# Optimization experiments

Measured on AMD Instinct MI355X. Metric: run time of the kernel, lower is better.

## Reference

```python
import jax, jax.numpy as jnp
import numpy as np

B, L, D, H = 8, 2048, 1024, 16
FACTOR = 3


def setup_inputs() -> dict:
    key = jax.random.key(0)
    ks = jax.random.split(key, 11)
    s = 0.02
    mk = lambda k, shp: jax.random.normal(k, shp, dtype=jnp.float32)
    return {
        "queries": mk(ks[0], (B, L, D)),
        "keys": mk(ks[1], (B, L, D)),
        "values": mk(ks[2], (B, L, D)),
        "Wq": mk(ks[3], (D, D)) * s, "bq": jnp.zeros((D,), jnp.float32),
        "Wk": mk(ks[4], (D, D)) * s, "bk": jnp.zeros((D,), jnp.float32),
        "Wv": mk(ks[5], (D, D)) * s, "bv": jnp.zeros((D,), jnp.float32),
        "Wo": mk(ks[6], (D, D)) * s, "bo": jnp.zeros((D,), jnp.float32),
    }


def reference(queries, keys, values, Wq, bq, Wk, bk, Wv, bv, Wo, bo):
    b, length, d = queries.shape
    h = H
    e = d // h
    q = (queries @ Wq + bq).reshape(b, length, h, e)
    k = (keys @ Wk + bk).reshape(b, length, h, e)
    v = (values @ Wv + bv).reshape(b, length, h, e)

    # [B, H, E, L] layout for FFT along time
    qf = jnp.fft.rfft(q.transpose(0, 2, 3, 1), axis=-1)
    kf = jnp.fft.rfft(k.transpose(0, 2, 3, 1), axis=-1)
    corr = jnp.fft.irfft(qf * jnp.conj(kf), n=length, axis=-1)  # [B,H,E,L]

    vperm = v.transpose(0, 2, 3, 1)  # [B,H,E,L]
    top_k = int(FACTOR * np.log(length))  # static: 22 for L=2048
    weights, delay = jax.lax.top_k(corr, top_k)          # [B,H,E,K]
    temp_corr = jax.nn.softmax(weights, axis=-1)         # [B,H,E,K]

    idx0 = jnp.arange(length)  # [L]
    agg = jnp.zeros_like(vperm)
    # small fixed loop over top-k delays (mirrors original structure)
    for i in range(top_k):
        # faithful to source: indices wrapped mod 8 (original code quirk)
        td = (idx0[None, None, None, :] + delay[..., i:i + 1]) % 8  # [B,H,E,L]
        pattern = jnp.take_along_axis(vperm, td, axis=-1)
        agg = agg + pattern * temp_corr[..., i:i + 1]

    result = agg.transpose(0, 3, 1, 2).reshape(b, length, d)  # [B,L,D]
    out = result @ Wo + bo
    return (out, corr.transpose(0, 3, 1, 2))
```

## Files before the change

### kernel.cpp

```cpp
#include <hip/hip_runtime.h>
#include <cstdint>
#include <cstddef>


#define TOPK 22

typedef __attribute__((ext_vector_type(8))) short short8;
typedef __attribute__((ext_vector_type(4))) float f32x4;

__device__ __forceinline__ float bf2f(unsigned short u) {
  union { unsigned int i; float f; } w;
  w.i = ((unsigned int)u) << 16;
  return w.f;
}
__device__ __forceinline__ unsigned short f2bf(float f) {
  union { float f; unsigned int i; } w;
  w.f = f;
  unsigned int x = w.i;
  x += 0x7fffu + ((x >> 16) & 1u);
  return (unsigned short)(x >> 16);
}

__device__ __forceinline__ float2 make2(float x, float y) { float2 r; r.x = x; r.y = y; return r; }
__device__ __forceinline__ float2 cadd(float2 a, float2 b) { return make2(a.x + b.x, a.y + b.y); }
__device__ __forceinline__ float2 csub(float2 a, float2 b) { return make2(a.x - b.x, a.y - b.y); }
__device__ __forceinline__ float2 cmul(float2 a, float2 b) {
  return make2(a.x * b.x - a.y * b.y, a.x * b.y + a.y * b.x);
}

__device__ __forceinline__ int cfi(int u) { return 2 * u + (((u) >> 5) << 1); }

template <bool INV>
__device__ __forceinline__ void dft8(float2 (&v)[8]) {
  const float C = 0.70710678118654752f;
  float2 s0 = cadd(v[0], v[4]), s1 = csub(v[0], v[4]);
  float2 s2 = cadd(v[2], v[6]), s3 = csub(v[2], v[6]);
  float2 E0 = cadd(s0, s2), E2 = csub(s0, s2);
  float2 E1, E3;
  if (!INV) { E1 = make2(s1.x + s3.y, s1.y - s3.x); E3 = make2(s1.x - s3.y, s1.y + s3.x); }
  else      { E1 = make2(s1.x - s3.y, s1.y + s3.x); E3 = make2(s1.x + s3.y, s1.y - s3.x); }
  float2 q0 = cadd(v[1], v[5]), q1 = csub(v[1], v[5]);
  float2 q2 = cadd(v[3], v[7]), q3 = csub(v[3], v[7]);
  float2 O0 = cadd(q0, q2), O2 = csub(q0, q2);
  float2 O1, O3;
  if (!INV) { O1 = make2(q1.x + q3.y, q1.y - q3.x); O3 = make2(q1.x - q3.y, q1.y + q3.x); }
  else      { O1 = make2(q1.x - q3.y, q1.y + q3.x); O3 = make2(q1.x + q3.y, q1.y - q3.x); }
  float2 T0 = O0, T1, T2, T3;
  if (!INV) {
    T1 = make2(C * (O1.x + O1.y), C * (O1.y - O1.x));
    T2 = make2(O2.y, -O2.x);
    T3 = make2(C * (O3.y - O3.x), -C * (O3.x + O3.y));
  } else {
    T1 = make2(C * (O1.x - O1.y), C * (O1.x + O1.y));
    T2 = make2(-O2.y, O2.x);
    T3 = make2(-C * (O3.x + O3.y), C * (O3.x - O3.y));
  }
  v[0] = cadd(E0, T0); v[4] = csub(E0, T0);
  v[1] = cadd(E1, T1); v[5] = csub(E1, T1);
  v[2] = cadd(E2, T2); v[6] = csub(E2, T2);
  v[3] = cadd(E3, T3); v[7] = csub(E3, T3);
}

template <bool INV>
__device__ __forceinline__ void dft4(float2 (&v)[4]) {
  float2 s0 = cadd(v[0], v[2]), s1 = csub(v[0], v[2]);
  float2 s2 = cadd(v[1], v[3]), s3 = csub(v[1], v[3]);
  v[0] = cadd(s0, s2); v[2] = csub(s0, s2);
  if (!INV) { v[1] = make2(s1.x + s3.y, s1.y - s3.x); v[3] = make2(s1.x - s3.y, s1.y + s3.x); }
  else      { v[1] = make2(s1.x - s3.y, s1.y + s3.x); v[3] = make2(s1.x + s3.y, s1.y - s3.x); }
}

template <int NS, bool INV>
__device__ __forceinline__ void stage8(const float* __restrict__ src,
                                       float* __restrict__ dst, int tid) {
  float2 v[8];
#pragma unroll
  for (int m = 0; m < 8; ++m)
    v[m] = *reinterpret_cast<const float2*>(src + cfi(tid + (m << 8)));
  if constexpr (NS > 1) {
    const int r = tid & (NS - 1);
    const float rev = (INV ? (1.0f / (8 * NS)) : (-1.0f / (8 * NS))) * (float)r;
    float2 w1; w1.x = __builtin_amdgcn_cosf(rev); w1.y = __builtin_amdgcn_sinf(rev);
    const float2 w2 = cmul(w1, w1);
    const float2 w3 = cmul(w2, w1);
    const float2 w4 = cmul(w2, w2);
    const float2 w5 = cmul(w4, w1);
    const float2 w6 = cmul(w4, w2);
    const float2 w7 = cmul(w4, w3);
    v[1] = cmul(v[1], w1); v[2] = cmul(v[2], w2); v[3] = cmul(v[3], w3);
    v[4] = cmul(v[4], w4); v[5] = cmul(v[5], w5); v[6] = cmul(v[6], w6);
    v[7] = cmul(v[7], w7);
  }
  dft8<INV>(v);
  const int r2 = tid & (NS - 1);
  const int d = ((tid & ~(NS - 1)) << 3) | r2;
#pragma unroll
  for (int m = 0; m < 8; ++m)
    *reinterpret_cast<float2*>(dst + cfi(d + m * NS)) = v[m];
}

__device__ __forceinline__ void radix_pick(const unsigned int* h,
                                           unsigned int* sb,
                                           unsigned int need, int tid) {
  if (tid < 64) {
    const unsigned int c0 = h[4 * tid + 0];
    const unsigned int c1 = h[4 * tid + 1];
    const unsigned int c2 = h[4 * tid + 2];
    const unsigned int c3 = h[4 * tid + 3];
    const unsigned int g = c0 + c1 + c2 + c3;
    unsigned int S = g;
#pragma unroll
    for (int off = 1; off < 64; off <<= 1) {
      const unsigned int o = __shfl_down(S, off);
      if (tid + off < 64) S += o;
    }
    unsigned int A = S - g;
    int pick = -1;
    unsigned int nn = 0;
    const unsigned int cc[4] = {c0, c1, c2, c3};
#pragma unroll
    for (int j = 3; j >= 0; --j) {
      if (pick < 0) {
        if (A < need && need <= A + cc[j]) { pick = j; nn = need - A; }
        else A += cc[j];
      }
    }
    if (pick >= 0) { sb[0] = (unsigned int)(4 * tid + pick); sb[1] = nn; }
  }
}

__global__ __launch_bounds__(256) void transpose_w(
    const float* __restrict__ Wq, const float* __restrict__ Wk,
    unsigned short* __restrict__ WqT, unsigned short* __restrict__ WkT) {
  __shared__ unsigned short T[64][72];
  const float* src = blockIdx.z ? Wk : Wq;
  unsigned short* dst = blockIdx.z ? WkT : WqT;
  const int k0 = blockIdx.x * 64;
  const int n0 = blockIdx.y * 64;
  const int c = threadIdx.x & 63;
  const int r0 = threadIdx.x >> 6;
#pragma unroll
  for (int p = 0; p < 16; ++p) {
    const int r = r0 + 4 * p;
    T[c][r] = f2bf(src[(size_t)(k0 + r) * 1024 + n0 + c]);
  }
  __syncthreads();
#pragma unroll
  for (int p = 0; p < 16; ++p) {
    const int nn = r0 + 4 * p;
    dst[(size_t)(n0 + nn) * 1024 + k0 + c] = T[nn][c];
  }
}

__global__ __launch_bounds__(256, 2) void gemm_qk(
    const float* __restrict__ A,
    const unsigned short* __restrict__ WT,
    const float* __restrict__ bias,
    unsigned short* __restrict__ outT) {
  __shared__ __align__(16) unsigned short smem[16384];
  unsigned short* As = smem;
  unsigned short* Bs = smem + 4096;

  const int tid = threadIdx.x;
  const int lane = tid & 63;
  const int w = tid >> 6;
  const int wr = w >> 1, wc = w & 1;
  const int m0 = blockIdx.x * 128;
  const int n0 = blockIdx.y * 128;
  const int l15 = lane & 15;
  const int quad = lane >> 4;

  f32x4 acc[4][4];
#pragma unroll
  for (int i = 0; i < 4; ++i)
#pragma unroll
    for (int j = 0; j < 4; ++j)
#pragma unroll
      for (int r = 0; r < 4; ++r) acc[i][j][r] = 0.f;

  for (int k0 = 0; k0 < 1024; k0 += 32) {
    __syncthreads();
#pragma unroll
    for (int h = 0; h < 2; ++h) {
      const int c = tid + h * 256;
      const int row = c >> 2;
      const int kc = (c & 3) * 8;
      const float* ap = A + (size_t)(m0 + row) * 1024 + k0 + kc;
      const float4 a0 = *reinterpret_cast<const float4*>(ap);
      const float4 a1 = *reinterpret_cast<const float4*>(ap + 4);
      uint4 pa;
      pa.x = f2bf(a0.x) | ((unsigned int)f2bf(a0.y) << 16);
      pa.y = f2bf(a0.z) | ((unsigned int)f2bf(a0.w) << 16);
      pa.z = f2bf(a1.x) | ((unsigned int)f2bf(a1.y) << 16);
      pa.w = f2bf(a1.z) | ((unsigned int)f2bf(a1.w) << 16);
      *reinterpret_cast<uint4*>(As + row * 32 + kc) = pa;
      uint4 vb = *reinterpret_cast<const uint4*>(WT + (size_t)(n0 + row) * 1024 + k0 + kc);
      *reinterpret_cast<uint4*>(Bs + row * 32 + kc) = vb;
    }
    __syncthreads();

    short8 af[4], bfr[4];
#pragma unroll
    for (int mt = 0; mt < 4; ++mt)
      af[mt] = *reinterpret_cast<const short8*>(As + (wr * 64 + mt * 16 + l15) * 32 + quad * 8);
#pragma unroll
    for (int nt = 0; nt < 4; ++nt)
      bfr[nt] = *reinterpret_cast<const short8*>(Bs + (wc * 64 + nt * 16 + l15) * 32 + quad * 8);
#pragma unroll
    for (int mt = 0; mt < 4; ++mt)
#pragma unroll
      for (int nt = 0; nt < 4; ++nt)
        acc[mt][nt] = __builtin_amdgcn_mfma_f32_16x16x32_bf16(af[mt], bfr[nt], acc[mt][nt], 0, 0, 0);
  }

  __syncthreads();
  unsigned short* Cs = smem;
#pragma unroll
  for (int nt = 0; nt < 4; ++nt) {
    const int n_local = wc * 64 + nt * 16 + l15;
    const float bv = bias[n0 + n_local];
#pragma unroll
    for (int mt = 0; mt < 4; ++mt) {
      const int mbase = wr * 64 + mt * 16 + quad * 4;
#pragma unroll
      for (int r = 0; r < 4; ++r)
        Cs[n_local * 128 + mbase + r] = f2bf(acc[mt][nt][r] + bv);
    }
  }
  __syncthreads();

  const int b = m0 >> 11;
  const int l0 = m0 & 2047;
  for (int it = tid; it < 2048; it += 256) {
    const int rowi = it >> 4;
    const int ci = it & 15;
    uint4 v = *reinterpret_cast<const uint4*>(Cs + rowi * 128 + ci * 8);
    *reinterpret_cast<uint4*>(outT + (size_t)(b * 1024 + n0 + rowi) * 2048 + l0 + ci * 8) = v;
  }
}

__global__ __launch_bounds__(256) void vsmall_kernel(
    const float* __restrict__ values,
    const float* __restrict__ Wv,
    const float* __restrict__ bv,
    float* __restrict__ out) {
  __shared__ float xr[1024];
  const int m = blockIdx.x;
  const int b = m >> 3, t = m & 7;
  const float* row = values + ((size_t)b * 2048 + t) * 1024;
  for (int i = threadIdx.x; i < 1024; i += 256) xr[i] = row[i];
  __syncthreads();
  const int n = blockIdx.y * 256 + threadIdx.x;
  float acc = 0.f;
#pragma unroll 8
  for (int k = 0; k < 1024; ++k) acc += xr[k] * Wv[(size_t)k * 1024 + n];
  out[(size_t)m * 1024 + n] = acc + bv[n];
}

__global__ __launch_bounds__(256, 4) void corr_topk(
    const unsigned short* __restrict__ Qt,
    const unsigned short* Kt,
    const float* __restrict__ vsmall,
    unsigned short* corrOut,
    float* __restrict__ agg) {
  __shared__ __align__(16) float bufA[4224];
  __shared__ __align__(16) float bufB[4224];

  const int tid = threadIdx.x;
  const int lane = tid & 63;
  const int wv = tid >> 6;
  const int s = blockIdx.x;
  const size_t base = (size_t)s * 2048;

  unsigned int* hist = reinterpret_cast<unsigned int*>(bufB);
  float* bins = bufB + 1024;
  float* wred = bufB + 1032;
  int* ired = reinterpret_cast<int*>(bufB + 1036);
  unsigned int* sb = reinterpret_cast<unsigned int*>(bufB + 1040);

  {
    float2 v[8];
#pragma unroll
    for (int m = 0; m < 8; ++m) {
      const int u = tid + (m << 8);
      v[m] = make2(bf2f(Qt[base + u]), bf2f(Kt[base + u]));
    }
    dft8<false>(v);
    const int d = tid << 3;
#pragma unroll
    for (int m = 0; m < 8; ++m)
      *reinterpret_cast<float2*>(bufA + cfi(d + m)) = v[m];
  }
  __syncthreads();

  stage8<8, false>(bufA, bufB, tid);
  __syncthreads();
  stage8<64, false>(bufB, bufA, tid);
  __syncthreads();

  {
#pragma unroll
    for (int h = 0; h < 2; ++h) {
      const int j = tid + (h << 8);
      float2 v[4];
#pragma unroll
      for (int m = 0; m < 4; ++m)
        v[m] = *reinterpret_cast<const float2*>(bufA + cfi(j + (m << 9)));
      const float rev = -(1.0f / 2048.0f) * (float)j;
      float2 w1; w1.x = __builtin_amdgcn_cosf(rev); w1.y = __builtin_amdgcn_sinf(rev);
      const float2 w2 = cmul(w1, w1);
      const float2 w3 = cmul(w2, w1);
      v[1] = cmul(v[1], w1); v[2] = cmul(v[2], w2); v[3] = cmul(v[3], w3);
      dft4<false>(v);
#pragma unroll
      for (int m = 0; m < 4; ++m)
        *reinterpret_cast<float2*>(bufB + cfi(j + (m << 9))) = v[m];
    }
  }
  __syncthreads();

  {
    float2 v[8];
    const float ks = 1.0f / 8192.0f;
#pragma unroll
    for (int m = 0; m < 8; ++m) {
      const int u = tid + (m << 8);
      const int ub = (2048 - u) & 2047;
      const float2 Av = *reinterpret_cast<const float2*>(bufB + cfi(u));
      const float2 Bv = *reinterpret_cast<const float2*>(bufB + cfi(ub));
      const float Px = Av.x + Bv.x, Py = Av.y - Bv.y;
      const float Qx = Av.x - Bv.x, Qy = -Av.y - Bv.y;
      const float X1 = (Px * Qx - Py * Qy) * ks;
      const float Y1 = (Px * Qy + Py * Qx) * ks;
      v[m] = make2(-Y1, X1);
    }
    dft8<true>(v);
    const int d = tid << 3;
#pragma unroll
    for (int m = 0; m < 8; ++m)
      *reinterpret_cast<float2*>(bufA + cfi(d + m)) = v[m];
  }
  __syncthreads();

  stage8<8, true>(bufA, bufB, tid);
  __syncthreads();
  stage8<64, true>(bufB, bufA, tid);
  __syncthreads();

  float cval[8];
#pragma unroll
  for (int h = 0; h < 2; ++h) {
    const int j = tid + (h << 8);
    float2 v0 = *reinterpret_cast<const float2*>(bufA + cfi(j));
    float2 v1 = *reinterpret_cast<const float2*>(bufA + cfi(j + 512));
    float2 v2 = *reinterpret_cast<const float2*>(bufA + cfi(j + 1024));
    float2 v3 = *reinterpret_cast<const float2*>(bufA + cfi(j + 1536));
    const float rev = (1.0f / 2048.0f) * (float)j;
    float2 w1; w1.x = __builtin_amdgcn_cosf(rev); w1.y = __builtin_amdgcn_sinf(rev);
    const float2 w2 = cmul(w1, w1);
    const float2 w3 = cmul(w2, w1);
    const float2 t1 = cmul(v1, w1);
    const float2 t3 = cmul(v3, w3);
    const float t2x = v2.x * w2.x - v2.y * w2.y;
    cval[h]     = v0.x + t1.x + t2x + t3.x;
    cval[h + 2] = v0.x - t1.y - t2x + t3.y;
    cval[h + 4] = v0.x - t1.x + t2x - t3.x;
    cval[h + 6] = v0.x + t1.y - t2x - t3.y;
  }

#pragma unroll
  for (int i = 0; i < 8; ++i)
    corrOut[base + (size_t)(tid + (i << 8))] = f2bf(cval[i]);

  unsigned int key[8];
#pragma unroll
  for (int i = 0; i < 8; ++i) {
    union { float f; unsigned int u; } cvt;
    cvt.f = cval[i];
    const unsigned int b = cvt.u;
    key[i] = (b & 0x80000000u) ? ~b : (b | 0x80000000u);
  }

#pragma unroll
  for (int q = 0; q < 4; ++q) hist[(q << 8) + tid] = 0u;
  if (tid < 8) bins[tid] = 0.f;
  {
    float vm = cval[0];
#pragma unroll
    for (int i = 1; i < 8; ++i) vm = fmaxf(vm, cval[i]);
#pragma unroll
    for (int off = 32; off > 0; off >>= 1) vm = fmaxf(vm, __shfl_down(vm, off));
    if (lane == 0) wred[wv] = vm;
  }
  __syncthreads();
  const float mx = fmaxf(fmaxf(wred[0], wred[1]), fmaxf(wred[2], wred[3]));

  unsigned int prefix = 0;
  unsigned int need = TOPK;
#pragma unroll
  for (int i = 0; i < 8; ++i) atomicAdd(&hist[key[i] >> 24], 1u);
  __syncthreads();
  radix_pick(hist, sb, need, tid);
  __syncthreads();
  prefix = sb[0]; need = sb[1];
#pragma unroll
  for (int i = 0; i < 8; ++i)
    if ((key[i] >> 24) == prefix) atomicAdd(&hist[256 + ((key[i] >> 16) & 255u)], 1u);
  __syncthreads();
  radix_pick(hist + 256, sb, need, tid);
  __syncthreads();
  prefix = (prefix << 8) | sb[0]; need = sb[1];
#pragma unroll
  for (int i = 0; i < 8; ++i)
    if ((key[i] >> 16) == prefix) atomicAdd(&hist[512 + ((key[i] >> 8) & 255u)], 1u);
  __syncthreads();
  radix_pick(hist + 512, sb, need, tid);
  __syncthreads();
  prefix = (prefix << 8) | sb[0]; need = sb[1];
#pragma unroll
  for (int i = 0; i < 8; ++i)
    if ((key[i] >> 8) == prefix) atomicAdd(&hist[768 + (key[i] & 255u)], 1u);
  __syncthreads();
  radix_pick(hist + 768, sb, need, tid);
  __syncthreads();
  const unsigned int T = (prefix << 8) | sb[0];
  const unsigned int takeEq = sb[1];

  unsigned int eqm = 0, selEq = 0;
#pragma unroll
  for (int i = 0; i < 8; ++i)
    if (key[i] == T) eqm |= (1u << i);
  for (unsigned int it2 = 0; it2 < takeEq; ++it2) {
    int mi = 0x7fffffff;
#pragma unroll
    for (int i = 0; i < 8; ++i)
      if (eqm & (1u << i)) mi = min(mi, tid + (i << 8));
#pragma unroll
    for (int off = 32; off > 0; off >>= 1) {
      const int o = __shfl_down(mi, off);
      if (lane + off < 64) mi = min(mi, o);
    }
    if (lane == 0) ired[wv] = mi;
    __syncthreads();
    const int gm = min(min(ired[0], ired[1]), min(ired[2], ired[3]));
#pragma unroll
    for (int i = 0; i < 8; ++i)
      if ((tid + (i << 8)) == gm) { selEq |= (1u << i); eqm &= ~(1u << i); }
    if (it2 + 1 < takeEq) __syncthreads();
  }

  float esum = 0.f;
#pragma unroll
  for (int i = 0; i < 8; ++i) {
    const bool sel = (key[i] > T) || ((selEq >> i) & 1u);
    if (sel) esum += __expf(cval[i] - mx);
  }
  if (esum > 0.f) atomicAdd(&bins[tid & 7], esum);
  __syncthreads();

  if (tid < 8) {
    const float ssum = bins[0] + bins[1] + bins[2] + bins[3] +
                       bins[4] + bins[5] + bins[6] + bins[7];
    const int b = s >> 10, n = s & 1023;
    float a = 0.f;
#pragma unroll
    for (int c = 0; c < 8; ++c)
      a += bins[c] * vsmall[(size_t)(b * 8 + ((tid + c) & 7)) * 1024 + n];
    agg[(size_t)(b * 8 + tid) * 1024 + n] = a / ssum;
  }
}

__global__ __launch_bounds__(256) void osmall_kernel(
    const float* __restrict__ aggin,
    const float* __restrict__ Wo,
    const float* __restrict__ bo,
    float* __restrict__ out) {
  __shared__ float xr[1024];
  const int m = blockIdx.x;
  const float* row = aggin + (size_t)m * 1024;
  for (int i = threadIdx.x; i < 1024; i += 256) xr[i] = row[i];
  __syncthreads();
  const int n = blockIdx.y * 256 + threadIdx.x;
  float acc = 0.f;
#pragma unroll 8
  for (int k = 0; k < 1024; ++k) acc += xr[k] * Wo[(size_t)k * 1024 + n];
  out[(size_t)m * 1024 + n] = acc + bo[n];
}

__global__ __launch_bounds__(256) void corr_transpose(
    const unsigned short* __restrict__ corrWs,
    float* __restrict__ out1) {
  __shared__ unsigned short T[64][72];
  const int bb = blockIdx.z;
  const int l0 = blockIdx.x * 64;
  const int n0 = blockIdx.y * 64;
  const int c = threadIdx.x & 63;
  const int r0 = threadIdx.x >> 6;
#pragma unroll
  for (int p = 0; p < 16; ++p) {
    const int r = r0 + 4 * p;
    T[c][r] = corrWs[(size_t)(bb * 1024 + n0 + r) * 2048 + l0 + c];
  }
  __syncthreads();
#pragma unroll
  for (int p = 0; p < 16; ++p) {
    const int ll = r0 + 4 * p;
    out1[(size_t)(bb * 2048 + l0 + ll) * 1024 + n0 + c] = bf2f(T[ll][c]);
  }
}

__global__ __launch_bounds__(256) void bcast_out(
    const float* __restrict__ outSmall,
    float* __restrict__ out0) {
  const size_t i4 = (size_t)blockIdx.x * 256 + threadIdx.x;
  const size_t basee = i4 * 4;
  const int n = (int)(basee & 1023);
  const int l = (int)((basee >> 10) & 2047);
  const int b = (int)(basee >> 21);
  const float4 v = *reinterpret_cast<const float4*>(outSmall + ((size_t)(b * 8 + (l & 7)) << 10) + n);
  *reinterpret_cast<float4*>(out0 + basee) = v;
}

extern "C" void kernel_launch(void* const* d_in, const int* in_sizes, int n_in,
                              void* d_out, int out_size, void* d_ws, size_t ws_size,
                              hipStream_t stream) {
  const float* queries = (const float*)d_in[0];
  const float* keys    = (const float*)d_in[1];
  const float* values  = (const float*)d_in[2];
  const float* Wq = (const float*)d_in[3];
  const float* bq = (const float*)d_in[4];
  const float* Wk = (const float*)d_in[5];
  const float* bk = (const float*)d_in[6];
  const float* Wv = (const float*)d_in[7];
  const float* bv = (const float*)d_in[8];
  const float* Wo = (const float*)d_in[9];
  const float* bo = (const float*)d_in[10];

  char* ws = (char*)d_ws;
  unsigned short* WqT = (unsigned short*)(ws);
  unsigned short* WkT = (unsigned short*)(ws + (2u << 20));
  unsigned short* Qt  = (unsigned short*)(ws + (4u << 20));
  float* vsmall   = (float*)(ws + (36u << 20));
  float* aggbuf   = (float*)(ws + (36u << 20) + (256u << 10));
  float* outSmall = (float*)(ws + (36u << 20) + (512u << 10));

  float* out0 = (float*)d_out;
  float* out1 = out0 + (size_t)16777216;
  unsigned short* Kt = (unsigned short*)d_out;
  unsigned short* corrWs = Kt;

  transpose_w<<<dim3(16, 16, 2), 256, 0, stream>>>(Wq, Wk, WqT, WkT);
  gemm_qk<<<dim3(128, 8), 256, 0, stream>>>(queries, WqT, bq, Qt);
  gemm_qk<<<dim3(128, 8), 256, 0, stream>>>(keys, WkT, bk, Kt);
  vsmall_kernel<<<dim3(64, 4), 256, 0, stream>>>(values, Wv, bv, vsmall);
  corr_topk<<<8192, 256, 0, stream>>>(Qt, Kt, vsmall, corrWs, aggbuf);
  osmall_kernel<<<dim3(64, 4), 256, 0, stream>>>(aggbuf, Wo, bo, outSmall);
  corr_transpose<<<dim3(32, 16, 8), 256, 0, stream>>>(corrWs, out1);
  bcast_out<<<16384, 256, 0, stream>>>(outSmall, out0);
}
```

Measured before the change: 611.5 us.

## Pre-convert Q/K inputs to bf16 and stage GEMM tiles via direct global-to-LDS loads

Adds a separate pass that converts the fp32 queries and keys to bf16 into scratch space carved from the output buffer. The projection GEMM then reads bf16 A tiles and uses global_load_lds to copy A and B tiles straight into shared memory. This removes the fp32 reads and in-loop conversion that each GEMM block repeated over its A rows across 8 column blocks, and takes the register round-trip out of LDS staging. The cost is an extra kernel launch plus a full write and re-read of 64 MB of bf16 data, and the new load-to-LDS tile layout has to match the fragment read pattern.

```diff
diff --git a/kernel.cpp b/kernel.cpp
--- a/kernel.cpp
+++ b/kernel.cpp
@@ -19,6 +19,12 @@
   unsigned int x = w.i;
   x += 0x7fffu + ((x >> 16) & 1u);
   return (unsigned short)(x >> 16);
+}
+
+__device__ __forceinline__ void gload_lds16(const void* g, void* l) {
+  __builtin_amdgcn_global_load_lds(
+      (const __attribute__((address_space(1))) unsigned int*)g,
+      (__attribute__((address_space(3))) unsigned int*)l, 16, 0, 0);
 }
 
 __device__ __forceinline__ float2 make2(float x, float y) { float2 r; r.x = x; r.y = y; return r; }
@@ -129,6 +135,27 @@
   }
 }
 
+__global__ __launch_bounds__(256) void conv_bf16(
+    const float* __restrict__ q, const float* __restrict__ k,
+    unsigned short* __restrict__ qb, unsigned short* __restrict__ kb) {
+  const size_t nchunks = (size_t)16777216 / 8;
+  for (size_t i = (size_t)blockIdx.x * 256 + threadIdx.x; i < 2 * nchunks;
+       i += (size_t)gridDim.x * 256) {
+    const bool isq = i < nchunks;
+    const float* src = isq ? q : k;
+    unsigned short* dst = isq ? qb : kb;
+    const size_t c = isq ? i : i - nchunks;
+    const float4 a0 = reinterpret_cast<const float4*>(src)[c * 2];
+    const float4 a1 = reinterpret_cast<const float4*>(src)[c * 2 + 1];
+    uint4 p;
+    p.x = f2bf(a0.x) | ((unsigned int)f2bf(a0.y) << 16);
+    p.y = f2bf(a0.z) | ((unsigned int)f2bf(a0.w) << 16);
+    p.z = f2bf(a1.x) | ((unsigned int)f2bf(a1.y) << 16);
+    p.w = f2bf(a1.z) | ((unsigned int)f2bf(a1.w) << 16);
+    reinterpret_cast<uint4*>(dst)[c] = p;
+  }
+}
+
 __global__ __launch_bounds__(256) void transpose_w(
     const float* __restrict__ Wq, const float* __restrict__ Wk,
     unsigned short* __restrict__ WqT, unsigned short* __restrict__ WkT) {
@@ -152,8 +179,8 @@
   }
 }
 
-__global__ __launch_bounds__(256, 2) void gemm_qk(
-    const float* __restrict__ A,
+__global__ __launch_bounds__(256, 2) void gemm_qk_bf(
+    const unsigned short* __restrict__ Abf,
     const unsigned short* __restrict__ WT,
     const float* __restrict__ bias,
     unsigned short* __restrict__ outT) {
@@ -170,6 +197,9 @@
   const int l15 = lane & 15;
   const int quad = lane >> 4;
 
+  const int srow = lane >> 2;
+  const int scol = (lane & 3) * 8;
+
   f32x4 acc[4][4];
 #pragma unroll
   for (int i = 0; i < 4; ++i)
@@ -180,22 +210,14 @@
 
   for (int k0 = 0; k0 < 1024; k0 += 32) {
     __syncthreads();
-#pragma unroll
-    for (int h = 0; h < 2; ++h) {
-      const int c = tid + h * 256;
-      const int row = c >> 2;
-      const int kc = (c & 3) * 8;
-      const float* ap = A + (size_t)(m0 + row) * 1024 + k0 + kc;
-      const float4 a0 = *reinterpret_cast<const float4*>(ap);
-      const float4 a1 = *reinterpret_cast<const float4*>(ap + 4);
-      uint4 pa;
-      pa.x = f2bf(a0.x) | ((unsigned int)f2bf(a0.y) << 16);
-      pa.y = f2bf(a0.z) | ((unsigned int)f2bf(a0.w) << 16);
-      pa.z = f2bf(a1.x) | ((unsigned int)f2bf(a1.y) << 16);
-      pa.w = f2bf(a1.z) | ((unsigned int)f2bf(a1.w) << 16);
-      *reinterpret_cast<uint4*>(As + row * 32 + kc) = pa;
-      uint4 vb = *reinterpret_cast<const uint4*>(WT + (size_t)(n0 + row) * 1024 + k0 + kc);
-      *reinterpret_cast<uint4*>(Bs + row * 32 + kc) = vb;
+    const unsigned short* Ab = Abf + (size_t)m0 * 1024 + k0;
+    const unsigned short* Bb = WT + (size_t)n0 * 1024 + k0;
+#pragma unroll
+    for (int i = 0; i < 2; ++i) {
+      const int cc = w * 2 + i;
+      const int row = cc * 16 + srow;
+      gload_lds16(Ab + (size_t)row * 1024 + scol, As + cc * 512);
+      gload_lds16(Bb + (size_t)row * 1024 + scol, Bs + cc * 512);
     }
     __syncthreads();
 
@@ -548,10 +570,13 @@
   float* out1 = out0 + (size_t)16777216;
   unsigned short* Kt = (unsigned short*)d_out;
   unsigned short* corrWs = Kt;
-
+  unsigned short* Qbf = (unsigned short*)out1;
+  unsigned short* Kbf = Qbf + (size_t)16777216;
+
+  conv_bf16<<<4096, 256, 0, stream>>>(queries, keys, Qbf, Kbf);
   transpose_w<<<dim3(16, 16, 2), 256, 0, stream>>>(Wq, Wk, WqT, WkT);
-  gemm_qk<<<dim3(128, 8), 256, 0, stream>>>(queries, WqT, bq, Qt);
-  gemm_qk<<<dim3(128, 8), 256, 0, stream>>>(keys, WkT, bk, Kt);
+  gemm_qk_bf<<<dim3(128, 8), 256, 0, stream>>>(Qbf, WqT, bq, Qt);
+  gemm_qk_bf<<<dim3(128, 8), 256, 0, stream>>>(Kbf, WkT, bk, Kt);
   vsmall_kernel<<<dim3(64, 4), 256, 0, stream>>>(values, Wv, bv, vsmall);
   corr_topk<<<8192, 256, 0, stream>>>(Qt, Kt, vsmall, corrWs, aggbuf);
   osmall_kernel<<<dim3(64, 4), 256, 0, stream>>>(aggbuf, Wo, bo, outSmall);
```

After: 632.5 us. +3.4%, slower.

## Merge Q/K projection launches and fuse output projection with broadcast store

Applied to the files above, without the earlier changes.

The Q and K projection GEMMs now run as one launch, with blockIdx.z selecting the input, weight, bias and output pointers. This removes a launch and lets the two grids share the tail. The small Wo projection and the broadcast of its 8-row-periodic result into the full [B,L,D] output are fused into one kernel, so the intermediate outSmall buffer and one launch go away. In exchange, the 64 MB output write is now issued by only 256 blocks, each thread doing 256 scalar strided stores. Before, 16384 blocks wrote it with float4 stores, so the fused version may not saturate write bandwidth.

```diff
diff --git a/kernel.cpp b/kernel.cpp
--- a/kernel.cpp
+++ b/kernel.cpp
@@ -153,13 +153,19 @@
 }
 
 __global__ __launch_bounds__(256, 2) void gemm_qk(
-    const float* __restrict__ A,
-    const unsigned short* __restrict__ WT,
-    const float* __restrict__ bias,
-    unsigned short* __restrict__ outT) {
+    const float* __restrict__ Aq, const float* __restrict__ Ak,
+    const unsigned short* __restrict__ WqT, const unsigned short* __restrict__ WkT,
+    const float* __restrict__ bq, const float* __restrict__ bk,
+    unsigned short* __restrict__ outQ, unsigned short* __restrict__ outK) {
   __shared__ __align__(16) unsigned short smem[16384];
   unsigned short* As = smem;
   unsigned short* Bs = smem + 4096;
+
+  const int z = blockIdx.z;
+  const float* A = z ? Ak : Aq;
+  const unsigned short* WT = z ? WkT : WqT;
+  const float* bias = z ? bk : bq;
+  unsigned short* outT = z ? outK : outQ;
 
   const int tid = threadIdx.x;
   const int lane = tid & 63;
@@ -470,23 +476,6 @@
   }
 }
 
-__global__ __launch_bounds__(256) void osmall_kernel(
-    const float* __restrict__ aggin,
-    const float* __restrict__ Wo,
-    const float* __restrict__ bo,
-    float* __restrict__ out) {
-  __shared__ float xr[1024];
-  const int m = blockIdx.x;
-  const float* row = aggin + (size_t)m * 1024;
-  for (int i = threadIdx.x; i < 1024; i += 256) xr[i] = row[i];
-  __syncthreads();
-  const int n = blockIdx.y * 256 + threadIdx.x;
-  float acc = 0.f;
-#pragma unroll 8
-  for (int k = 0; k < 1024; ++k) acc += xr[k] * Wo[(size_t)k * 1024 + n];
-  out[(size_t)m * 1024 + n] = acc + bo[n];
-}
-
 __global__ __launch_bounds__(256) void corr_transpose(
     const unsigned short* __restrict__ corrWs,
     float* __restrict__ out1) {
@@ -509,16 +498,26 @@
   }
 }
 
-__global__ __launch_bounds__(256) void bcast_out(
-    const float* __restrict__ outSmall,
+__global__ __launch_bounds__(256) void osmall_bcast(
+    const float* __restrict__ aggin,
+    const float* __restrict__ Wo,
+    const float* __restrict__ bo,
     float* __restrict__ out0) {
-  const size_t i4 = (size_t)blockIdx.x * 256 + threadIdx.x;
-  const size_t basee = i4 * 4;
-  const int n = (int)(basee & 1023);
-  const int l = (int)((basee >> 10) & 2047);
-  const int b = (int)(basee >> 21);
-  const float4 v = *reinterpret_cast<const float4*>(outSmall + ((size_t)(b * 8 + (l & 7)) << 10) + n);
-  *reinterpret_cast<float4*>(out0 + basee) = v;
+  __shared__ float xr[1024];
+  const int m = blockIdx.x;
+  const int b = m >> 3, t = m & 7;
+  const float* row = aggin + (size_t)m * 1024;
+  for (int i = threadIdx.x; i < 1024; i += 256) xr[i] = row[i];
+  __syncthreads();
+  const int n = blockIdx.y * 256 + threadIdx.x;
+  float acc = 0.f;
+#pragma unroll 8
+  for (int k = 0; k < 1024; ++k) acc += xr[k] * Wo[(size_t)k * 1024 + n];
+  acc += bo[n];
+  float* o = out0 + ((size_t)b * 2048 + t) * 1024 + n;
+#pragma unroll 4
+  for (int l8 = 0; l8 < 256; ++l8)
+    o[(size_t)l8 * 8192] = acc;
 }
 
 extern "C" void kernel_launch(void* const* d_in, const int* in_sizes, int n_in,
@@ -542,7 +541,6 @@
   unsigned short* Qt  = (unsigned short*)(ws + (4u << 20));
   float* vsmall   = (float*)(ws + (36u << 20));
   float* aggbuf   = (float*)(ws + (36u << 20) + (256u << 10));
-  float* outSmall = (float*)(ws + (36u << 20) + (512u << 10));
 
   float* out0 = (float*)d_out;
   float* out1 = out0 + (size_t)16777216;
@@ -550,11 +548,9 @@
   unsigned short* corrWs = Kt;
 
   transpose_w<<<dim3(16, 16, 2), 256, 0, stream>>>(Wq, Wk, WqT, WkT);
-  gemm_qk<<<dim3(128, 8), 256, 0, stream>>>(queries, WqT, bq, Qt);
-  gemm_qk<<<dim3(128, 8), 256, 0, stream>>>(keys, WkT, bk, Kt);
+  gemm_qk<<<dim3(128, 8, 2), 256, 0, stream>>>(queries, keys, WqT, WkT, bq, bk, Qt, Kt);
   vsmall_kernel<<<dim3(64, 4), 256, 0, stream>>>(values, Wv, bv, vsmall);
   corr_topk<<<8192, 256, 0, stream>>>(Qt, Kt, vsmall, corrWs, aggbuf);
-  osmall_kernel<<<dim3(64, 4), 256, 0, stream>>>(aggbuf, Wo, bo, outSmall);
   corr_transpose<<<dim3(32, 16, 8), 256, 0, stream>>>(corrWs, out1);
-  bcast_out<<<16384, 256, 0, stream>>>(outSmall, out0);
-}
+  osmall_bcast<<<dim3(64, 4), 256, 0, stream>>>(aggbuf, Wo, bo, out0);
+}
```

Result: no change. 610.2 us (-0.2%).
